# Kernel optimization log

Hardware: AMD Instinct MI355X
Metric: run time of the kernel (lower is better)

## Reference

```python
import jax, jax.numpy as jnp
import numpy as np

H = 1024       # hidden_size
NH = 16        # num heads
HD = H // NH   # head dim
EPS = 1e-12


def setup_inputs() -> dict:
    key = jax.random.key(0)
    ks = jax.random.split(key, 12)
    s = 1.0 / np.sqrt(H)
    return {
        "hidden_states": jax.random.normal(ks[0], (2, 2048, H), jnp.float32),
        "attention_mask": jnp.zeros((2, 1, 1, 2048), jnp.float32),
        "wq": jax.random.uniform(ks[1], (H, H), jnp.float32, -s, s),
        "bq": jnp.zeros((H,), jnp.float32),
        "wk": jax.random.uniform(ks[2], (H, H), jnp.float32, -s, s),
        "bk": jnp.zeros((H,), jnp.float32),
        "wv": jax.random.uniform(ks[3], (H, H), jnp.float32, -s, s),
        "bv": jnp.zeros((H,), jnp.float32),
        "wo": jax.random.uniform(ks[4], (H, H), jnp.float32, -s, s),
        "bo": jnp.zeros((H,), jnp.float32),
        "ln_gamma": jnp.ones((H,), jnp.float32),
        "ln_beta": jnp.zeros((H,), jnp.float32),
    }


def reference(hidden_states, attention_mask, wq, bq, wk, bk, wv, bv, wo, bo, ln_gamma, ln_beta):
    residual = hidden_states
    # pre-LayerNorm
    mu = jnp.mean(hidden_states, axis=-1, keepdims=True)
    var = jnp.var(hidden_states, axis=-1, keepdims=True)
    x = (hidden_states - mu) / jnp.sqrt(var + EPS) * ln_gamma + ln_beta

    B, S, _ = x.shape
    # QKV projections (torch Linear: x @ W.T + b), split heads -> [B, NH, S, HD]
    def proj(w, b):
        return (x @ w.T + b).reshape(B, S, NH, HD).transpose(0, 2, 1, 3)
    q = proj(wq, bq)
    k = proj(wk, bk)
    v = proj(wv, bv)

    scores = jnp.einsum("bhqd,bhkd->bhqk", q, k) / np.sqrt(HD).astype(np.float32)
    scores = scores + attention_mask  # broadcast additive mask
    probs = jax.nn.softmax(scores, axis=-1)
    ctx = jnp.einsum("bhqk,bhkd->bhqd", probs, v)
    ctx = ctx.transpose(0, 2, 1, 3).reshape(B, S, NH * HD)

    out = ctx @ wo.T + bo
    return out + residual
```

## Files before the change

### kernel.cpp

```cpp
#include <hip/hip_runtime.h>
#include <cstdint>

typedef unsigned short u16;
typedef __bf16  bf16x8 __attribute__((ext_vector_type(8)));
typedef unsigned short u16x8 __attribute__((ext_vector_type(8)));
typedef unsigned short u16x4 __attribute__((ext_vector_type(4)));
typedef float   f32x4  __attribute__((ext_vector_type(4)));

#define LOG2E 1.44269504088896340736f

__device__ __forceinline__ u16 f2b(float f) {
  union { __bf16 h; u16 u; } c; c.h = (__bf16)f;
  return c.u;
}

__device__ __forceinline__ int swz(int row) { return (row & 7) ^ ((row >> 3) & 7); }
__device__ __forceinline__ int sidx(int row, int k) {
  return row * 64 + ((((k >> 3) ^ swz(row)) & 7) << 3) + (k & 7);
}
__device__ __forceinline__ bf16x8 ld_frag(const u16* base, int row, int k) {
  return *(const bf16x8*)(base + sidx(row, k));
}

__device__ __forceinline__ void async16(const u16* g, u16* l) {
  __builtin_amdgcn_global_load_lds(
      (__attribute__((address_space(1))) unsigned int*)(uintptr_t)g,
      (__attribute__((address_space(3))) unsigned int*)(uintptr_t)l,
      16, 0, 0);
}

__global__ __launch_bounds__(256) void cvt_kernel(
    const float* __restrict__ w0, const float* __restrict__ w1,
    const float* __restrict__ w2, const float* __restrict__ w3,
    u16* __restrict__ dst) {
  const float* src = (blockIdx.y == 0) ? w0 : (blockIdx.y == 1) ? w1
                   : (blockIdx.y == 2) ? w2 : w3;
  const int idx = (blockIdx.x * 256 + threadIdx.x) * 4;
  f32x4 v = *(const f32x4*)(src + idx);
  u16x4 o;
#pragma unroll
  for (int j = 0; j < 4; ++j) o[j] = f2b(v[j]);
  *(u16x4*)(dst + (size_t)blockIdx.y * 1048576 + idx) = o;
}

__global__ __launch_bounds__(256) void ln_kernel(
    const float* __restrict__ hs, const float* __restrict__ gamma,
    const float* __restrict__ beta, u16* __restrict__ X) {
  __shared__ float red[8];
  const int row = blockIdx.x;
  const int tid = threadIdx.x;
  f32x4 v = *(const f32x4*)(hs + (size_t)row * 1024 + tid * 4);
  float s = 0.f, s2 = 0.f;
#pragma unroll
  for (int j = 0; j < 4; ++j) { s += v[j]; s2 += v[j] * v[j]; }
#pragma unroll
  for (int o = 1; o < 64; o <<= 1) { s += __shfl_xor(s, o); s2 += __shfl_xor(s2, o); }
  const int wid = tid >> 6, lane = tid & 63;
  if (lane == 0) { red[wid] = s; red[4 + wid] = s2; }
  __syncthreads();
  s  = red[0] + red[1] + red[2] + red[3];
  s2 = red[4] + red[5] + red[6] + red[7];
  const float mean = s * (1.f / 1024.f);
  const float var  = fmaxf(s2 * (1.f / 1024.f) - mean * mean, 0.f);
  const float rstd = rsqrtf(var + 1e-12f);
  f32x4 g = *(const f32x4*)(gamma + tid * 4);
  f32x4 bb = *(const f32x4*)(beta + tid * 4);
  u16x4 outv;
#pragma unroll
  for (int j = 0; j < 4; ++j) outv[j] = f2b((v[j] - mean) * rstd * g[j] + bb[j]);
  *(u16x4*)(X + (size_t)row * 1024 + tid * 4) = outv;
}

template <int MODE>
__device__ __forceinline__ void gemm_tile_128(
    const u16* __restrict__ A, const u16* __restrict__ Bt,
    const float* __restrict__ bias, const float* __restrict__ res,
    void* __restrict__ Cv, int ldc, int m0, int nG) {
  __shared__ __align__(16) u16 As[128 * 64];
  __shared__ __align__(16) u16 Bs[128 * 64];
  const int tid = threadIdx.x;
  const int wid = tid >> 6;
  const int lane = tid & 63;
  const int l15 = lane & 15, lq = lane >> 4;
  const int wm = (wid & 1) << 6, wn = (wid >> 1) << 6;
  const int srow = tid >> 3;
  const int sg = tid & 7;

  f32x4 acc[4][4] = {};

  for (int k0 = 0; k0 < 1024; k0 += 64) {
#pragma unroll
    for (int i = 0; i < 4; ++i) {
      int row = (i << 5) + srow;
      int kc  = k0 + (((sg ^ swz(row)) & 7) << 3);
      async16(A + (size_t)row * 1024 + kc, As + (i << 11) + (wid << 9));
    }
#pragma unroll
    for (int i = 0; i < 4; ++i) {
      int row = (i << 5) + srow;
      int kc  = k0 + (((sg ^ swz(row)) & 7) << 3);
      async16(Bt + (size_t)row * 1024 + kc, Bs + (i << 11) + (wid << 9));
    }
    __syncthreads();
#pragma unroll
    for (int kk = 0; kk < 2; ++kk) {
      bf16x8 af[4], bf[4];
#pragma unroll
      for (int mi = 0; mi < 4; ++mi) af[mi] = ld_frag(As, wm + (mi << 4) + l15, (kk << 5) + (lq << 3));
#pragma unroll
      for (int ni = 0; ni < 4; ++ni) bf[ni] = ld_frag(Bs, wn + (ni << 4) + l15, (kk << 5) + (lq << 3));
#pragma unroll
      for (int mi = 0; mi < 4; ++mi)
#pragma unroll
        for (int ni = 0; ni < 4; ++ni)
          acc[mi][ni] = __builtin_amdgcn_mfma_f32_16x16x32_bf16(af[mi], bf[ni], acc[mi][ni], 0, 0, 0);
    }
    __syncthreads();
  }
#pragma unroll
  for (int ni = 0; ni < 4; ++ni) {
    const int n = wn + (ni << 4) + l15;
    const float bv = bias[n];
    if (MODE == 2) {
      const int ng = nG + n, hh = ng >> 6, dd = ng & 63;
#pragma unroll
      for (int mi = 0; mi < 4; ++mi) {
        const int mbase = wm + (mi << 4) + (lq << 2);
        u16x4 pk;
#pragma unroll
        for (int r = 0; r < 4; ++r) pk[r] = f2b(acc[mi][ni][r] + bv);
        const int mg = m0 + mbase;
        const int bb = mg >> 11, ss = mg & 2047;
        *(u16x4*)((u16*)Cv + ((size_t)((bb << 4) + hh) * 64 + dd) * 2048 + ss) = pk;
      }
    } else {
#pragma unroll
      for (int mi = 0; mi < 4; ++mi) {
#pragma unroll
        for (int r = 0; r < 4; ++r) {
          const int m = wm + (mi << 4) + (lq << 2) + r;
          float v = acc[mi][ni][r] + bv;
          if (MODE == 1) {
            v += res[(size_t)m * ldc + n];
            ((float*)Cv)[(size_t)m * ldc + n] = v;
          } else {
            ((u16*)Cv)[(size_t)m * ldc + n] = f2b(v);
          }
        }
      }
    }
  }
}

__global__ __launch_bounds__(256, 2) void qkv_kernel(
    const u16* __restrict__ X, const u16* __restrict__ W,
    const float* __restrict__ bq, const float* __restrict__ bk, const float* __restrict__ bv,
    u16* __restrict__ QK, u16* __restrict__ VT) {
  const int n0 = blockIdx.x << 7;
  const int m0 = blockIdx.y << 7;
  const int wsel = n0 >> 10;
  const int nloc = n0 & 1023;
  const u16* Bt = W + (size_t)wsel * 1048576 + (size_t)nloc * 1024;
  if (wsel < 2) {
    const float* bias = (wsel == 0 ? bq : bk) + nloc;
    gemm_tile_128<0>(X + (size_t)m0 * 1024, Bt, bias, nullptr,
                     QK + (size_t)m0 * 2048 + n0, 2048, 0, 0);
  } else {
    gemm_tile_128<2>(X + (size_t)m0 * 1024, Bt, bv + nloc, nullptr,
                     VT, 0, m0, nloc);
  }
}

__global__ __launch_bounds__(256, 2) void out_kernel(
    const u16* __restrict__ CTX, const u16* __restrict__ wo,
    const float* __restrict__ bo, const float* __restrict__ res, float* __restrict__ OUT) {
  const int n0 = blockIdx.x << 7;
  const int m0 = blockIdx.y << 7;
  gemm_tile_128<1>(CTX + (size_t)m0 * 1024, wo + (size_t)n0 * 1024, bo + n0,
                   res + (size_t)m0 * 1024 + n0, OUT + (size_t)m0 * 1024 + n0, 1024, 0, 0);
}

__global__ __launch_bounds__(512, 2) void attn_kernel(
    const u16* __restrict__ QK, const u16* __restrict__ VT,
    const float* __restrict__ mask, u16* __restrict__ CTX) {
  __shared__ __align__(16) u16 Ksb[2][64 * 64];
  __shared__ __align__(16) u16 Vtsb[2][64 * 64];
  __shared__ __align__(16) u16 Ps[8 * 32 * 64];
  const int tid = threadIdx.x;
  const int wid = tid >> 6;
  const int lane = tid & 63;
  const int l15 = lane & 15, lq = lane >> 4;
  const int qt = blockIdx.x, h = blockIdx.y, b = blockIdx.z;

  const int qbase = (b << 11) + (qt << 8) + (wid << 5);
  const u16* Kbase  = QK + (size_t)(b << 11) * 2048 + 1024 + (h << 6);
  const u16* VTbase = VT + (size_t)(((b << 4) + h) << 6) * 2048;

  bf16x8 qf[2][2];
#pragma unroll
  for (int f = 0; f < 2; ++f)
#pragma unroll
    for (int kc = 0; kc < 2; ++kc)
      qf[f][kc] = *(const bf16x8*)(QK + (size_t)(qbase + (f << 4) + l15) * 2048 + (h << 6) + (kc << 5) + (lq << 3));

  f32x4 cacc[2][4] = {};
  float m_run[2] = {-1.0e30f, -1.0e30f}, l_run[2] = {0.f, 0.f};

  const int strow = (wid << 3) + (lane >> 3);
  const int sg = lane & 7;
  const int gko = ((sg ^ swz(strow)) & 7) << 3;
  u16* Pw = Ps + (wid << 11);

  async16(Kbase + (size_t)strow * 2048 + gko, &Ksb[0][0] + (wid << 9));
  async16(VTbase + (size_t)strow * 2048 + gko, &Vtsb[0][0] + (wid << 9));

  for (int kt = 0; kt < 32; ++kt) {
    const u16* Ks  = &Ksb[kt & 1][0];
    const u16* Vts = &Vtsb[kt & 1][0];
    __syncthreads();
    if (kt + 1 < 32) {
      u16* Kd = &Ksb[(kt + 1) & 1][0] + (wid << 9);
      u16* Vd = &Vtsb[(kt + 1) & 1][0] + (wid << 9);
      async16(Kbase + (size_t)(((kt + 1) << 6) + strow) * 2048 + gko, Kd);
      async16(VTbase + (size_t)strow * 2048 + ((kt + 1) << 6) + gko, Vd);
    }

    f32x4 sacc[2][4] = {};
#pragma unroll
    for (int kc = 0; kc < 2; ++kc) {
      bf16x8 kf[4];
#pragma unroll
      for (int ki = 0; ki < 4; ++ki) kf[ki] = ld_frag(Ks, (ki << 4) + l15, (kc << 5) + (lq << 3));
#pragma unroll
      for (int f = 0; f < 2; ++f)
#pragma unroll
        for (int ki = 0; ki < 4; ++ki)
          sacc[f][ki] = __builtin_amdgcn_mfma_f32_16x16x32_bf16(kf[ki], qf[f][kc], sacc[f][ki], 0, 0, 0);
    }

    f32x4 mvl[4];
#pragma unroll
    for (int ki = 0; ki < 4; ++ki) {
      f32x4 mv = *(const f32x4*)(mask + (b << 11) + (kt << 6) + (ki << 4) + (lq << 2));
#pragma unroll
      for (int r = 0; r < 4; ++r) mvl[ki][r] = mv[r] * LOG2E;
    }

#pragma unroll
    for (int f = 0; f < 2; ++f) {
      float tm = -1.0e30f;
#pragma unroll
      for (int ki = 0; ki < 4; ++ki)
#pragma unroll
        for (int r = 0; r < 4; ++r) {
          float sv = sacc[f][ki][r] * (0.125f * LOG2E) + mvl[ki][r];
          sacc[f][ki][r] = sv;
          tm = fmaxf(tm, sv);
        }
      tm = fmaxf(tm, __shfl_xor(tm, 16));
      tm = fmaxf(tm, __shfl_xor(tm, 32));
      const float mnew  = fmaxf(m_run[f], tm);
      const float alpha = __builtin_amdgcn_exp2f(m_run[f] - mnew);
      float rs = 0.f;
#pragma unroll
      for (int ki = 0; ki < 4; ++ki)
#pragma unroll
        for (int r = 0; r < 4; ++r) {
          float pv = __builtin_amdgcn_exp2f(sacc[f][ki][r] - mnew);
          sacc[f][ki][r] = pv;
          rs += pv;
        }
      rs += __shfl_xor(rs, 16);
      rs += __shfl_xor(rs, 32);
      l_run[f] = l_run[f] * alpha + rs;
      m_run[f] = mnew;
#pragma unroll
      for (int dm = 0; dm < 4; ++dm)
#pragma unroll
        for (int r = 0; r < 4; ++r) cacc[f][dm][r] *= alpha;

#pragma unroll
      for (int ki = 0; ki < 4; ++ki) {
        u16x4 pk;
#pragma unroll
        for (int r = 0; r < 4; ++r) pk[r] = f2b(sacc[f][ki][r]);
        *(u16x4*)(Pw + sidx((f << 4) + l15, (ki << 4) + (lq << 2))) = pk;
      }
    }
    __asm__ volatile("" ::: "memory");

#pragma unroll
    for (int kc = 0; kc < 2; ++kc) {
      bf16x8 pf[2];
#pragma unroll
      for (int f = 0; f < 2; ++f) pf[f] = ld_frag(Pw, (f << 4) + l15, (kc << 5) + (lq << 3));
#pragma unroll
      for (int dm = 0; dm < 4; ++dm) {
        bf16x8 vf = ld_frag(Vts, (dm << 4) + l15, (kc << 5) + (lq << 3));
#pragma unroll
        for (int f = 0; f < 2; ++f)
          cacc[f][dm] = __builtin_amdgcn_mfma_f32_16x16x32_bf16(vf, pf[f], cacc[f][dm], 0, 0, 0);
      }
    }
  }

#pragma unroll
  for (int f = 0; f < 2; ++f) {
    const float inv = 1.0f / l_run[f];
    u16* Crow = CTX + (size_t)(qbase + (f << 4) + l15) * 1024 + (h << 6);
#pragma unroll
    for (int dm = 0; dm < 4; ++dm) {
      u16x4 o;
#pragma unroll
      for (int r = 0; r < 4; ++r) o[r] = f2b(cacc[f][dm][r] * inv);
      *(u16x4*)(Crow + (dm << 4) + (lq << 2)) = o;
    }
  }
}

extern "C" void kernel_launch(void* const* d_in, const int* in_sizes, int n_in,
                              void* d_out, int out_size, void* d_ws, size_t ws_size,
                              hipStream_t stream) {
  const float* hs   = (const float*)d_in[0];
  const float* mask = (const float*)d_in[1];
  const float* wq   = (const float*)d_in[2];
  const float* bq   = (const float*)d_in[3];
  const float* wk   = (const float*)d_in[4];
  const float* bk   = (const float*)d_in[5];
  const float* wv   = (const float*)d_in[6];
  const float* bv   = (const float*)d_in[7];
  const float* wo   = (const float*)d_in[8];
  const float* bo   = (const float*)d_in[9];
  const float* lg   = (const float*)d_in[10];
  const float* lb   = (const float*)d_in[11];

  u16* X   = (u16*)d_ws;
  u16* QK  = X + (size_t)4096 * 1024;
  u16* CTX = QK + (size_t)4096 * 2048;
  u16* W   = CTX + (size_t)4096 * 1024;
  u16* VT  = W + (size_t)4 * 1048576;
  float* OUT = (float*)d_out;

  ln_kernel<<<4096, 256, 0, stream>>>(hs, lg, lb, X);
  cvt_kernel<<<dim3(1024, 4), 256, 0, stream>>>(wq, wk, wv, wo, W);
  qkv_kernel<<<dim3(24, 32), 256, 0, stream>>>(X, W, bq, bk, bv, QK, VT);
  attn_kernel<<<dim3(8, 16, 2), 512, 0, stream>>>(QK, VT, mask, CTX);
  out_kernel<<<dim3(8, 32), 256, 0, stream>>>(CTX, W + (size_t)3 * 1048576, bo, hs, OUT);
}
```

Measured before the change: 239.6 us.

## Split attention over KV halves and merge partial results; raise occupancy bounds

Attention now splits the key sequence into two halves across extra blocks, doubling the grid from 256 to 512 blocks. Each half writes a normalized partial context plus its running max and sum, and a new merge kernel combines the two halves with log-sum-exp weights. Launch bounds for the GEMM and attention kernels are raised to request higher occupancy. This aims to fill more compute units during attention, at the cost of an extra kernel launch, partial-result traffic, rounding the partials to bf16, and possible register spills.

```diff
diff --git a/kernel.cpp b/kernel.cpp
--- a/kernel.cpp
+++ b/kernel.cpp
@@ -12,6 +12,9 @@
 __device__ __forceinline__ u16 f2b(float f) {
   union { __bf16 h; u16 u; } c; c.h = (__bf16)f;
   return c.u;
+}
+__device__ __forceinline__ float b2f(u16 u) {
+  union { unsigned int i; float f; } c; c.i = ((unsigned int)u) << 16; return c.f;
 }
 
 __device__ __forceinline__ int swz(int row) { return (row & 7) ^ ((row >> 3) & 7); }
@@ -152,7 +155,7 @@
   }
 }
 
-__global__ __launch_bounds__(256, 2) void qkv_kernel(
+__global__ __launch_bounds__(256, 3) void qkv_kernel(
     const u16* __restrict__ X, const u16* __restrict__ W,
     const float* __restrict__ bq, const float* __restrict__ bk, const float* __restrict__ bv,
     u16* __restrict__ QK, u16* __restrict__ VT) {
@@ -171,7 +174,7 @@
   }
 }
 
-__global__ __launch_bounds__(256, 2) void out_kernel(
+__global__ __launch_bounds__(256, 3) void out_kernel(
     const u16* __restrict__ CTX, const u16* __restrict__ wo,
     const float* __restrict__ bo, const float* __restrict__ res, float* __restrict__ OUT) {
   const int n0 = blockIdx.x << 7;
@@ -180,9 +183,9 @@
                    res + (size_t)m0 * 1024 + n0, OUT + (size_t)m0 * 1024 + n0, 1024, 0, 0);
 }
 
-__global__ __launch_bounds__(512, 2) void attn_kernel(
+__global__ __launch_bounds__(512, 4) void attn_kernel(
     const u16* __restrict__ QK, const u16* __restrict__ VT,
-    const float* __restrict__ mask, u16* __restrict__ CTX) {
+    const float* __restrict__ mask, u16* __restrict__ PCTX, float2* __restrict__ ML) {
   __shared__ __align__(16) u16 Ksb[2][64 * 64];
   __shared__ __align__(16) u16 Vtsb[2][64 * 64];
   __shared__ __align__(16) u16 Ps[8 * 32 * 64];
@@ -190,9 +193,11 @@
   const int wid = tid >> 6;
   const int lane = tid & 63;
   const int l15 = lane & 15, lq = lane >> 4;
-  const int qt = blockIdx.x, h = blockIdx.y, b = blockIdx.z;
-
-  const int qbase = (b << 11) + (qt << 8) + (wid << 5);
+  const int qt = blockIdx.x, h = blockIdx.y, bz = blockIdx.z;
+  const int b = bz >> 1, sp = bz & 1;
+  const int kt0 = sp << 4, kt1 = kt0 + 16;
+
+  const int qloc = (qt << 8) + (wid << 5);
   const u16* Kbase  = QK + (size_t)(b << 11) * 2048 + 1024 + (h << 6);
   const u16* VTbase = VT + (size_t)(((b << 4) + h) << 6) * 2048;
 
@@ -201,7 +206,7 @@
   for (int f = 0; f < 2; ++f)
 #pragma unroll
     for (int kc = 0; kc < 2; ++kc)
-      qf[f][kc] = *(const bf16x8*)(QK + (size_t)(qbase + (f << 4) + l15) * 2048 + (h << 6) + (kc << 5) + (lq << 3));
+      qf[f][kc] = *(const bf16x8*)(QK + (size_t)((b << 11) + qloc + (f << 4) + l15) * 2048 + (h << 6) + (kc << 5) + (lq << 3));
 
   f32x4 cacc[2][4] = {};
   float m_run[2] = {-1.0e30f, -1.0e30f}, l_run[2] = {0.f, 0.f};
@@ -211,14 +216,14 @@
   const int gko = ((sg ^ swz(strow)) & 7) << 3;
   u16* Pw = Ps + (wid << 11);
 
-  async16(Kbase + (size_t)strow * 2048 + gko, &Ksb[0][0] + (wid << 9));
-  async16(VTbase + (size_t)strow * 2048 + gko, &Vtsb[0][0] + (wid << 9));
-
-  for (int kt = 0; kt < 32; ++kt) {
+  async16(Kbase + (size_t)((kt0 << 6) + strow) * 2048 + gko, &Ksb[0][0] + (wid << 9));
+  async16(VTbase + (size_t)strow * 2048 + (kt0 << 6) + gko, &Vtsb[0][0] + (wid << 9));
+
+  for (int kt = kt0; kt < kt1; ++kt) {
     const u16* Ks  = &Ksb[kt & 1][0];
     const u16* Vts = &Vtsb[kt & 1][0];
     __syncthreads();
-    if (kt + 1 < 32) {
+    if (kt + 1 < kt1) {
       u16* Kd = &Ksb[(kt + 1) & 1][0] + (wid << 9);
       u16* Vd = &Vtsb[(kt + 1) & 1][0] + (wid << 9);
       async16(Kbase + (size_t)(((kt + 1) << 6) + strow) * 2048 + gko, Kd);
@@ -307,15 +312,44 @@
 #pragma unroll
   for (int f = 0; f < 2; ++f) {
     const float inv = 1.0f / l_run[f];
-    u16* Crow = CTX + (size_t)(qbase + (f << 4) + l15) * 1024 + (h << 6);
+    const int q = qloc + (f << 4) + l15;
+    const size_t base = ((size_t)((bz << 4) + h) * 2048 + q) * 64;
 #pragma unroll
     for (int dm = 0; dm < 4; ++dm) {
       u16x4 o;
 #pragma unroll
       for (int r = 0; r < 4; ++r) o[r] = f2b(cacc[f][dm][r] * inv);
-      *(u16x4*)(Crow + (dm << 4) + (lq << 2)) = o;
-    }
-  }
+      *(u16x4*)(PCTX + base + (dm << 4) + (lq << 2)) = o;
+    }
+    if (lq == 0) {
+      float2 ml; ml.x = m_run[f]; ml.y = l_run[f];
+      ML[(size_t)((bz << 4) + h) * 2048 + q] = ml;
+    }
+  }
+}
+
+__global__ __launch_bounds__(256) void merge_kernel(
+    const u16* __restrict__ PCTX, const float2* __restrict__ ML, u16* __restrict__ CTX) {
+  const int t = threadIdx.x;
+  const int hh = blockIdx.y;
+  const int b = hh >> 4, h = hh & 15;
+  const int q = (blockIdx.x << 4) + (t >> 4);
+  const int d = (t & 15) << 2;
+  const int bz0 = (b << 1), bz1 = bz0 + 1;
+  const size_t r0 = (size_t)((bz0 << 4) + h) * 2048 + q;
+  const size_t r1 = (size_t)((bz1 << 4) + h) * 2048 + q;
+  u16x4 p0 = *(const u16x4*)(PCTX + r0 * 64 + d);
+  u16x4 p1 = *(const u16x4*)(PCTX + r1 * 64 + d);
+  float2 ml0 = ML[r0], ml1 = ML[r1];
+  const float M = fmaxf(ml0.x, ml1.x);
+  const float a0 = __builtin_amdgcn_exp2f(ml0.x - M) * ml0.y;
+  const float a1 = __builtin_amdgcn_exp2f(ml1.x - M) * ml1.y;
+  const float rs = 1.0f / (a0 + a1);
+  const float w0 = a0 * rs, w1 = a1 * rs;
+  u16x4 o;
+#pragma unroll
+  for (int r = 0; r < 4; ++r) o[r] = f2b(b2f(p0[r]) * w0 + b2f(p1[r]) * w1);
+  *(u16x4*)(CTX + ((size_t)(b << 11) + q) * 1024 + (h << 6) + d) = o;
 }
 
 extern "C" void kernel_launch(void* const* d_in, const int* in_sizes, int n_in,
@@ -334,16 +368,19 @@
   const float* lg   = (const float*)d_in[10];
   const float* lb   = (const float*)d_in[11];
 
-  u16* X   = (u16*)d_ws;
-  u16* QK  = X + (size_t)4096 * 1024;
-  u16* CTX = QK + (size_t)4096 * 2048;
-  u16* W   = CTX + (size_t)4096 * 1024;
-  u16* VT  = W + (size_t)4 * 1048576;
+  u16* X    = (u16*)d_ws;
+  u16* QK   = X + (size_t)4096 * 1024;
+  u16* CTX  = QK + (size_t)4096 * 2048;
+  u16* W    = CTX + (size_t)4096 * 1024;
+  u16* VT   = W + (size_t)4 * 1048576;
+  u16* PCTX = VT + (size_t)4 * 1048576;
+  float2* ML = (float2*)(PCTX + (size_t)64 * 2048 * 64);
   float* OUT = (float*)d_out;
 
   ln_kernel<<<4096, 256, 0, stream>>>(hs, lg, lb, X);
   cvt_kernel<<<dim3(1024, 4), 256, 0, stream>>>(wq, wk, wv, wo, W);
   qkv_kernel<<<dim3(24, 32), 256, 0, stream>>>(X, W, bq, bk, bv, QK, VT);
-  attn_kernel<<<dim3(8, 16, 2), 512, 0, stream>>>(QK, VT, mask, CTX);
+  attn_kernel<<<dim3(8, 16, 4), 512, 0, stream>>>(QK, VT, mask, PCTX, ML);
+  merge_kernel<<<dim3(128, 32), 256, 0, stream>>>(PCTX, ML, CTX);
   out_kernel<<<dim3(8, 32), 256, 0, stream>>>(CTX, W + (size_t)3 * 1048576, bo, hs, OUT);
 }
```

New measurement: 336.6 us. 40.5% more time.
